# Kernel optimization log

Hardware: AMD Instinct MI355X
Metric: run time of the kernel (lower is better)

The kernel has to match this reference:

```python
import jax, jax.numpy as jnp
from jax import lax
import numpy as np

B = 2; C = 128; H = 128; W = 128; NPIX = H * W
HTH = 184; HTW = 180; NBINS = HTH * HTW
NSPH = 16384; KHT = 8; KSPH = 16
N0, N1, N2 = 1024, 256, 64
K0, K1, K2 = 8, 8, 8
EPS = 1e-5


def setup_inputs() -> dict:
    key = jax.random.key(0)
    ks = jax.random.split(key, 24)
    f32 = jnp.float32
    inp = {}
    inp["image"] = jax.random.normal(ks[0], (B, C, H, W), f32)
    inp["bn_gamma"] = jnp.ones((C,), f32)
    inp["bn_beta"] = jnp.zeros((C,), f32)
    inp["ht_idx"] = jax.random.randint(ks[1], (NBINS, KHT), 0, NPIX, jnp.int32)
    inp["ht_w"] = jax.random.uniform(ks[2], (NBINS, KHT), f32)
    inp["w_htconv"] = jax.random.normal(ks[3], (3, 3, C, C), f32) / np.sqrt(9.0 * C)
    inp["htbn_gamma"] = jnp.ones((C,), f32)
    inp["htbn_beta"] = jnp.zeros((C,), f32)
    inp["sph_idx"] = jax.random.randint(ks[4], (NSPH, KSPH), 0, NBINS, jnp.int32)
    inp["sph_w"] = jax.random.uniform(ks[5], (NSPH, KSPH), f32)
    inp["w_sc"] = jax.random.normal(ks[6], (3, 64, C), f32) / np.sqrt(1.0 * C)
    inp["b_sc"] = jnp.zeros((3, 64), f32)
    inp["scbn_gamma"] = jnp.ones((3, 64), f32)
    inp["scbn_beta"] = jnp.zeros((3, 64), f32)
    inp["dgcn_w"] = jax.random.normal(ks[7], (3, 4, 128, 64), f32) / np.sqrt(128.0)
    inp["dgcn_b"] = jnp.zeros((3, 4, 64), f32)
    inp["dgcn_hw"] = jax.random.normal(ks[8], (3, 64), f32) / 8.0
    inp["dgcn_hb"] = jnp.zeros((3,), f32)
    inp["ind0"] = jax.random.randint(ks[9], (B, N0), 0, NSPH, jnp.int32)
    inp["ind1"] = jax.random.randint(ks[10], (B, 3, N1), 0, NSPH, jnp.int32)
    inp["ind2"] = jax.random.randint(ks[11], (B, 3, N2), 0, NSPH, jnp.int32)
    # kNN-style edges: structured centers (each node repeated k times), random neighbors
    c0 = jnp.tile(jnp.repeat(jnp.arange(N0, dtype=jnp.int32), K0)[None], (B, 1))
    inp["edge0"] = jnp.stack([c0, jax.random.randint(ks[12], (B, N0 * K0), 0, N0, jnp.int32)], 1)
    c1 = jnp.broadcast_to(jnp.repeat(jnp.arange(N1, dtype=jnp.int32), K1)[None, None], (B, 3, N1 * K1))
    inp["edge1"] = jnp.stack([c1, jax.random.randint(ks[13], (B, 3, N1 * K1), 0, N1, jnp.int32)], 2)
    c2 = jnp.broadcast_to(jnp.repeat(jnp.arange(N2, dtype=jnp.int32), K2)[None, None], (B, 3, N2 * K2))
    inp["edge2"] = jnp.stack([c2, jax.random.randint(ks[14], (B, 3, N2 * K2), 0, N2, jnp.int32)], 2)
    inp["target0"] = jax.random.randint(ks[15], (B, N0), 0, 2, jnp.int32)
    inp["target1"] = jax.random.randint(ks[16], (B * 3, N1), 0, 2, jnp.int32)
    inp["target2"] = jax.random.randint(ks[17], (B * 3, N2), 0, 2, jnp.int32)
    return inp


def _bn2d(x, g, b):
    m = x.mean((0, 2, 3), keepdims=True)
    v = x.var((0, 2, 3), keepdims=True)
    return g[None, :, None, None] * (x - m) * lax.rsqrt(v + EPS) + b[None, :, None, None]


def _sphere(x_htf, sph_idx, sph_w, ind):
    # x_htf: [B,C,NBINS]; ind: [B,S] -> weighted gather of HT bins per sphere node
    mi = sph_idx[ind]          # [B,S,K]
    mw = sph_w[ind]            # [B,S,K]
    g = jax.vmap(lambda xb, ib: xb[:, ib])(x_htf, mi)   # [B,C,S,K]
    return (g * mw[:, None]).sum(-1)                    # [B,C,S]


def _sconv(x, w, b, g, be):
    # 1x1 conv [B,C,S]->[B,64,S] + BN1d (batch stats) + ReLU
    y = jnp.einsum('oc,bcs->bos', w, x) + b[None, :, None]
    m = y.mean((0, 2), keepdims=True)
    v = y.var((0, 2), keepdims=True)
    return jax.nn.relu(g[None, :, None] * (y - m) * lax.rsqrt(v + EPS) + be[None, :, None])


def _dgcn(x, edge, ws, bs, hw, hb, n, k):
    # x: [Bg,n,64]; edge: [Bg,2,n*k] (row0=center, row1=neighbor); 4 EdgeConv layers
    for i in range(4):
        xc = jnp.take_along_axis(x, edge[:, 0, :, None], axis=1)   # [Bg,n*k,Cin]
        xn = jnp.take_along_axis(x, edge[:, 1, :, None], axis=1)
        h = jax.nn.relu(jnp.concatenate([xc, xn - xc], -1) @ ws[i] + bs[i])
        x = h.reshape(x.shape[0], n, k, -1).max(2)                 # max over neighbors
    return x @ hw + hb                                             # [Bg,n] logits


def _bce(logits, target):
    t = target.astype(logits.dtype)
    l = jnp.maximum(logits, 0.0) - logits * t + jnp.log1p(jnp.exp(-jnp.abs(logits)))
    pos = t > 0.5
    npos = jnp.maximum(pos.sum(), 1).astype(l.dtype)
    nneg = jnp.maximum((~pos).sum(), 1).astype(l.dtype)
    return jnp.where(pos, l, 0.0).sum() / npos, jnp.where(pos, 0.0, l).sum() / nneg


def _forward(image, bn_gamma, bn_beta, ht_idx, ht_w, w_htconv, htbn_gamma, htbn_beta,
             sph_idx, sph_w, w_sc, b_sc, scbn_gamma, scbn_beta,
             dgcn_w, dgcn_b, dgcn_hw, dgcn_hb,
             ind0, ind1, ind2, edge0, edge1, edge2, target0, target1, target2):
    x = jax.nn.relu(_bn2d(image, bn_gamma, bn_beta))
    xf = x.reshape(B, C, NPIX)
    # Hough voting: each HT bin accumulates KHT weighted pixels
    ht = (xf[:, :, ht_idx] * ht_w).sum(-1).reshape(B, C, HTH, HTW)
    hc = lax.conv_general_dilated(ht, w_htconv, (1, 1), 'SAME',
                                  dimension_numbers=('NCHW', 'HWIO', 'NCHW'))
    x_htf = jax.nn.relu(_bn2d(hc, htbn_gamma, htbn_beta)).reshape(B, C, NBINS)

    # scale 0
    x0 = _sconv(_sphere(x_htf, sph_idx, sph_w, ind0),
                w_sc[0], b_sc[0], scbn_gamma[0], scbn_beta[0]).transpose(0, 2, 1)
    x0 = _dgcn(x0, edge0, dgcn_w[0], dgcn_b[0], dgcn_hw[0], dgcn_hb[0], N0, K0)   # [B,N0]
    # scale 1 (3 vanishing-point branches folded into batch)
    x1 = _sconv(_sphere(x_htf, sph_idx, sph_w, ind1.reshape(B, -1)),
                w_sc[1], b_sc[1], scbn_gamma[1], scbn_beta[1]).transpose(0, 2, 1)
    x1 = _dgcn(x1.reshape(B * 3, N1, 64), edge1.reshape(B * 3, 2, N1 * K1),
               dgcn_w[1], dgcn_b[1], dgcn_hw[1], dgcn_hb[1], N1, K1)              # [B*3,N1]
    # scale 2
    x2 = _sconv(_sphere(x_htf, sph_idx, sph_w, ind2.reshape(B, -1)),
                w_sc[2], b_sc[2], scbn_gamma[2], scbn_beta[2]).transpose(0, 2, 1)
    x2 = _dgcn(x2.reshape(B * 3, N2, 64), edge2.reshape(B * 3, 2, N2 * K2),
               dgcn_w[2], dgcn_b[2], dgcn_hw[2], dgcn_hb[2], N2, K2)              # [B*3,N2]

    lp0, ln0 = _bce(x0, target0)
    lp1, ln1 = _bce(x1, target1)
    lp2, ln2 = _bce(x2, target2)
    losses = jnp.stack([lp0, ln0, lp1, ln1, lp2, ln2])
    preds = jnp.concatenate([jax.nn.sigmoid(x0).reshape(B, -1),
                             jax.nn.sigmoid(x1).reshape(B, -1),
                             jax.nn.sigmoid(x2).reshape(B, -1)], axis=1)
    return losses, preds


def reference(image, bn_gamma, bn_beta, ht_idx, ht_w, w_htconv, htbn_gamma, htbn_beta,
              sph_idx, sph_w, w_sc, b_sc, scbn_gamma, scbn_beta,
              dgcn_w, dgcn_b, dgcn_hw, dgcn_hb,
              ind0, ind1, ind2, edge0, edge1, edge2, target0, target1, target2):
    return _forward(image, bn_gamma, bn_beta, ht_idx, ht_w, w_htconv, htbn_gamma, htbn_beta,
                    sph_idx, sph_w, w_sc, b_sc, scbn_gamma, scbn_beta,
                    dgcn_w, dgcn_b, dgcn_hw, dgcn_hb,
                    ind0, ind1, ind2, edge0, edge1, edge2, target0, target1, target2)
```

## Files before the change

kernel.cpp:

```cpp
#include <hip/hip_runtime.h>
#include <math.h>

#define B_ 2
#define C_ 128
#define NPIX_ 16384
#define HTH_ 184
#define HTW_ 180
#define NBINS_ 33120
#define PH_ 186
#define PW_ 184
#define NPB_ 1984
#define TOTN_ 3968
#define EPS_ 1e-5f

#define ST_HC_SUM 0
#define ST_HC_SQ  128
#define ST_SC_SUM 256
#define ST_SC_SQ  448
#define ST_LOSS   640
#define ST_IMG_S1 1472
#define ST_IMG_S2 1600

typedef __attribute__((ext_vector_type(8))) short v8s;
typedef __attribute__((ext_vector_type(4))) float v4f;

__device__ inline unsigned short f2b(float f) {
  unsigned u = __builtin_bit_cast(unsigned, f);
  unsigned r = u + 0x7fffu + ((u >> 16) & 1u);
  return (unsigned short)(r >> 16);
}
__device__ inline float b2f(unsigned short u) {
  unsigned v = ((unsigned)u) << 16;
  return __builtin_bit_cast(float, v);
}

__global__ void kprep0(const float* __restrict__ w, const float* __restrict__ dw,
                       const float* __restrict__ wsc,
                       unsigned short* __restrict__ wtb, unsigned short* __restrict__ dwb,
                       unsigned short* __restrict__ swb,
                       unsigned* __restrict__ htb2, const float* __restrict__ img,
                       float* __restrict__ st) {
  int bid = blockIdx.x;
  int tid = threadIdx.x;
  if (bid < 1612) {
    int idx = bid*256 + tid;
    if (idx < 147456) {
      int tap = idx >> 14, z = idx & 16383;
      int j = z & 7, lane = (z >> 3) & 63, nt = (z >> 9) & 7, kt = (z >> 12) & 3;
      int l = lane & 15, q = lane >> 4;
      int co = nt*16 + l, ci = kt*32 + q*8 + j;
      wtb[idx] = f2b(w[(tap*C_ + ci)*C_ + co]);
    } else if (idx < 245760) {
      int i2 = idx - 147456;
      int sl = i2 >> 13, z = i2 & 8191;
      int j = z & 7, lane = (z >> 3) & 63, nt = (z >> 9) & 3, kt = (z >> 11) & 3;
      int l = lane & 15, q = lane >> 4;
      int co = nt*16 + l, cc = kt*32 + q*8 + j;
      dwb[i2] = f2b(dw[(sl*128 + cc)*64 + co]);
    } else if (idx < 270336) {
      int i3 = idx - 245760;
      int s = i3 >> 13, z = i3 & 8191;
      int j = z & 7, lane = (z >> 3) & 63, nt = (z >> 9) & 3, kt = (z >> 11) & 3;
      int l = lane & 15, q = lane >> 4;
      int co = nt*16 + l, cc = kt*32 + q*8 + j;
      swb[i3] = f2b(wsc[(s*64 + co)*128 + cc]);
    } else if (idx < 412672) {
      int i = idx - 270336;
      int d = i & 63;
      int cell = i >> 6;
      int b = cell / 1112, j = cell % 1112;
      int y, x;
      if (j < 184) { y = 0; x = j; }
      else if (j < 368) { y = 185; x = j - 184; }
      else { int c = j - 368; int xi = c / 186; y = c % 186; x = xi == 0 ? 0 : 180 + xi; }
      htb2[((size_t)(b*PH_ + y)*PW_ + x)*64 + d] = 0u;
    }
  } else {
    int kb = bid - 1612;
    int c = kb >> 3, chunk = kb & 7;
    float s1 = 0.f, s2 = 0.f;
    for (int i = chunk*4096 + tid; i < (chunk+1)*4096; i += 256) {
      int b = i >> 14, p = i & (NPIX_-1);
      float v = img[((size_t)(b*C_ + c))*NPIX_ + p];
      s1 += v; s2 += v*v;
    }
    __shared__ float r1[256], r2[256];
    r1[tid] = s1; r2[tid] = s2; __syncthreads();
    for (int off = 128; off; off >>= 1) {
      if (tid < off) { r1[tid] += r1[tid+off]; r2[tid] += r2[tid+off]; }
      __syncthreads();
    }
    if (tid == 0) {
      atomicAdd(&st[ST_IMG_S1 + c], r1[0]);
      atomicAdd(&st[ST_IMG_S2 + c], r2[0]);
    }
  }
}

__global__ void k2_bnrelu_t(const float* __restrict__ img, const float* __restrict__ st,
                            const float* __restrict__ g, const float* __restrict__ be,
                            unsigned short* __restrict__ xt) {
  __shared__ float tile[32*65];
  __shared__ float ash[32], dsh[32];
  int p0 = blockIdx.x*64, c0 = blockIdx.y*32, b = blockIdx.z;
  int tid = threadIdx.x;
  if (tid < 32) {
    int c = c0 + tid;
    float n = (float)(B_*NPIX_);
    float m = st[ST_IMG_S1+c]/n;
    float var = st[ST_IMG_S2+c]/n - m*m;
    float a = g[c]*rsqrtf(var + EPS_);
    ash[tid] = a; dsh[tid] = be[c] - a*m;
  }
  __syncthreads();
  for (int r = 0; r < 8; r++) {
    int flat = tid + r*256;
    int row = flat >> 6, col = flat & 63;
    float v = img[((size_t)(b*C_ + c0 + row))*NPIX_ + p0 + col];
    tile[row*65 + col] = fmaxf(ash[row]*v + dsh[row], 0.f);
  }
  __syncthreads();
  for (int r = 0; r < 4; r++) {
    int flat = (tid + r*256)*2;
    int pl = flat >> 5, cl = flat & 31;
    unsigned lo = f2b(tile[cl*65 + pl]);
    unsigned hi = f2b(tile[(cl+1)*65 + pl]);
    *(unsigned*)&xt[((size_t)b*NPIX_ + p0 + pl)*C_ + c0 + cl] = lo | (hi << 16);
  }
}

__global__ void k3_hough(const unsigned* __restrict__ xt2, const int* __restrict__ hidx,
                         const float* __restrict__ hwt, unsigned* __restrict__ htb2) {
  int tid = threadIdx.x;
  int wv = __builtin_amdgcn_readfirstlane(tid >> 6);
  int bin = blockIdx.x*4 + wv;
  int b = blockIdx.y;
  int lane = tid & 63;
  const unsigned* base = xt2 + (size_t)b*NPIX_*64 + lane;
  float acc0 = 0.f, acc1 = 0.f;
  #pragma unroll
  for (int k = 0; k < 8; k++) {
    int p = hidx[bin*8 + k];
    float w = hwt[bin*8 + k];
    unsigned dv = base[(size_t)p*64];
    acc0 += w * b2f((unsigned short)(dv & 0xffff));
    acc1 += w * b2f((unsigned short)(dv >> 16));
  }
  int y = bin / HTW_, x = bin - y*HTW_;
  unsigned lo = f2b(acc0), hi = f2b(acc1);
  htb2[((size_t)(b*PH_ + y + 1)*PW_ + (x+1))*64 + lane] = lo | (hi << 16);
}

__global__ __launch_bounds__(256) void k4_mfma(
    const unsigned short* __restrict__ htb, const unsigned short* __restrict__ wtb,
    unsigned short* __restrict__ hcb, float* __restrict__ st) {
  __shared__ char smem[65536];
  int tid = threadIdx.x;
  int wav = tid >> 6, lane = tid & 63;
  int quad = lane >> 4, l16 = lane & 15;
  int b = blockIdx.y;
  int p0 = blockIdx.x*128 + wav*32;
  size_t ab[2];
  #pragma unroll
  for (int t = 0; t < 2; t++) {
    int px = p0 + t*16 + l16; if (px > NBINS_-1) px = NBINS_-1;
    int y = px / HTW_, x = px % HTW_;
    ab[t] = (((size_t)(b*PH_ + y))*PW_ + x)*C_ + quad*8;
  }
  v4f acc[2][8];
  #pragma unroll
  for (int t = 0; t < 2; t++)
    #pragma unroll
    for (int nt = 0; nt < 8; nt++) acc[t][nt] = (v4f){0,0,0,0};

  {
    const uint4* src = (const uint4*)wtb;
    uint4* dst = (uint4*)smem;
    #pragma unroll
    for (int s = 0; s < 8; s++) dst[tid + s*256] = src[tid + s*256];
  }
  __syncthreads();
  for (int tap = 0; tap < 9; tap++) {
    uint4 wreg[8];
    if (tap < 8) {
      const uint4* src = (const uint4*)(wtb + (tap+1)*16384);
      #pragma unroll
      for (int s = 0; s < 8; s++) wreg[s] = src[tid + s*256];
    }
    const char* cur = smem + (tap & 1)*32768;
    int dy = tap/3, dx = tap - dy*3;
    int toff = (dy*PW_ + dx)*C_;
    v8s a[2][4];
    #pragma unroll
    for (int t = 0; t < 2; t++)
      #pragma unroll
      for (int kt = 0; kt < 4; kt++)
        a[t][kt] = *(const v8s*)&htb[ab[t] + toff + kt*32];
    #pragma unroll
    for (int kt = 0; kt < 4; kt++) {
      #pragma unroll
      for (int nt = 0; nt < 8; nt++) {
        v8s bf = *(const v8s*)(cur + ((((kt*8 + nt)*64) + lane) << 4));
        acc[0][nt] = __builtin_amdgcn_mfma_f32_16x16x32_bf16(a[0][kt], bf, acc[0][nt], 0, 0, 0);
        acc[1][nt] = __builtin_amdgcn_mfma_f32_16x16x32_bf16(a[1][kt], bf, acc[1][nt], 0, 0, 0);
      }
    }
    if (tap < 8) {
      uint4* dst = (uint4*)(smem + ((tap+1) & 1)*32768);
      #pragma unroll
      for (int s = 0; s < 8; s++) dst[tid + s*256] = wreg[s];
    }
    __syncthreads();
  }
  float* red = (float*)smem;
  float s1[8], s2[8];
  #pragma unroll
  for (int nt = 0; nt < 8; nt++) { s1[nt] = 0.f; s2[nt] = 0.f; }
  #pragma unroll
  for (int t = 0; t < 2; t++) {
    int pbase = p0 + t*16 + quad*4;
    #pragma unroll
    for (int nt = 0; nt < 8; nt++) {
      int co = nt*16 + l16;
      #pragma unroll
      for (int reg = 0; reg < 4; reg++) {
        int po = pbase + reg;
        if (po < NBINS_) {
          float v = acc[t][nt][reg];
          hcb[((size_t)b*NBINS_ + po)*C_ + co] = f2b(v);
          s1[nt] += v; s2[nt] += v*v;
        }
      }
    }
  }
  int slot = wav*4 + quad;
  #pragma unroll
  for (int nt = 0; nt < 8; nt++) red[(nt*16 + l16)*17 + slot] = s1[nt];
  __syncthreads();
  if (tid < 128) {
    float s = 0.f;
    #pragma unroll
    for (int k = 0; k < 16; k++) s += red[tid*17 + k];
    atomicAdd(&st[ST_HC_SUM + tid], s);
  }
  __syncthreads();
  #pragma unroll
  for (int nt = 0; nt < 8; nt++) red[(nt*16 + l16)*17 + slot] = s2[nt];
  __syncthreads();
  if (tid < 128) {
    float s = 0.f;
    #pragma unroll
    for (int k = 0; k < 16; k++) s += red[tid*17 + k];
    atomicAdd(&st[ST_HC_SQ + tid], s);
  }
}

__global__ __launch_bounds__(256) void k67_sphconv(
    const unsigned* __restrict__ hcb2, const float* __restrict__ g, const float* __restrict__ be,
    const int* __restrict__ sph_idx, const float* __restrict__ sph_w,
    const int* __restrict__ ind0, const int* __restrict__ ind1, const int* __restrict__ ind2,
    const unsigned short* __restrict__ swb, const float* __restrict__ b_sc,
    float* __restrict__ y, float* __restrict__ st) {
  __shared__ unsigned short E[16*136];
  int tid = threadIdx.x;
  int gn0 = blockIdx.x*8;
  int nb0 = gn0 % NPB_;
  int s = nb0 < 1024 ? 0 : (nb0 < 1792 ? 1 : 2);
  int wv = tid >> 6, lane = tid & 63;
  int quad = lane >> 4, l16 = lane & 15;
  {
    int c0 = lane*2, c1 = c0 + 1;
    float n = (float)(B_*NBINS_);
    float m0 = st[ST_HC_SUM + c0]/n, m1 = st[ST_HC_SUM + c1]/n;
    float va0 = st[ST_HC_SQ + c0]/n - m0*m0, va1 = st[ST_HC_SQ + c1]/n - m1*m1;
    float a0 = g[c0]*rsqrtf(va0 + EPS_), a1 = g[c1]*rsqrtf(va1 + EPS_);
    float d0 = be[c0] - a0*m0, d1 = be[c1] - a1*m1;
    #pragma unroll
    for (int i = 0; i < 2; i++) {
      int node_l = wv*2 + i;
      int gn = gn0 + node_l;
      int b = gn / NPB_, nb = gn % NPB_;
      int v;
      if (nb < 1024) v = ind0[b*1024 + nb];
      else if (nb < 1792) v = ind1[b*768 + nb - 1024];
      else v = ind2[b*192 + nb - 1792];
      v = __builtin_amdgcn_readfirstlane(v);
      const unsigned* base = hcb2 + (size_t)b*NBINS_*64 + lane;
      float acc0 = 0.f, acc1 = 0.f;
      #pragma unroll
      for (int k = 0; k < 16; k++) {
        int mi = sph_idx[v*16 + k];
        float mw = sph_w[v*16 + k];
        unsigned dv = base[(size_t)mi*64];
        acc0 += mw * fmaxf(a0*b2f((unsigned short)(dv & 0xffff)) + d0, 0.f);
        acc1 += mw * fmaxf(a1*b2f((unsigned short)(dv >> 16)) + d1, 0.f);
      }
      unsigned lo = f2b(acc0), hi = f2b(acc1);
      *(unsigned*)&E[node_l*136 + c0] = lo | (hi << 16);
    }
  }
  __syncthreads();
  v4f acc = (v4f){0,0,0,0};
  const unsigned short* wb = swb + s*8192 + wv*512;
  #pragma unroll
  for (int kt = 0; kt < 4; kt++) {
    v8s a = *(const v8s*)&E[l16*136 + quad*8 + kt*32];
    v8s bf = *(const v8s*)&wb[kt*2048 + lane*8];
    acc = __builtin_amdgcn_mfma_f32_16x16x32_bf16(a, bf, acc, 0, 0, 0);
  }
  float bias = b_sc[s*64 + wv*16 + l16];
  float s1 = 0.f, s2 = 0.f;
  #pragma unroll
  for (int reg = 0; reg < 4; reg++) {
    int row = quad*4 + reg;
    if (quad < 2) {
      float val = acc[reg] + bias;
      y[(size_t)(gn0 + row)*64 + wv*16 + l16] = val;
      s1 += val; s2 += val*val;
    }
  }
  s1 += __shfl_xor(s1, 16);
  s2 += __shfl_xor(s2, 16);
  if (quad == 0) {
    atomicAdd(&st[ST_SC_SUM + s*64 + wv*16 + l16], s1);
    atomicAdd(&st[ST_SC_SQ  + s*64 + wv*16 + l16], s2);
  }
}

__global__ __launch_bounds__(256) void k10_dgcn(
    const void* __restrict__ xin_, unsigned short* __restrict__ xout,
    const int* __restrict__ edge0, const int* __restrict__ edge1, const int* __restrict__ edge2,
    const unsigned short* __restrict__ dwb, const float* __restrict__ db,
    const float* __restrict__ st, const float* __restrict__ scg, const float* __restrict__ scb,
    int layer, int usebn) {
  __shared__ unsigned short E[64*136];
  __shared__ float ash[64], dsh[64];
  int tid = threadIdx.x;
  int bid = blockIdx.x;
  int s, node_base, le_blk, span; const int* ec;
  if (bid < 256) {
    s = 0; int b = bid >> 7; node_base = b*NPB_; le_blk = (bid & 127)*64;
    span = 8192; ec = edge0 + b*2*8192;
  } else if (bid < 448) {
    int j = bid - 256; s = 1; int seg = j >> 5; int b = seg/3, vp = seg%3;
    node_base = b*NPB_ + 1024 + vp*256; le_blk = (j & 31)*64;
    span = 2048; ec = edge1 + ((b*3+vp)*2)*2048;
  } else {
    int j = bid - 448; s = 2; int seg = j >> 3; int b = seg/3, vp = seg%3;
    node_base = b*NPB_ + 1792 + vp*64; le_blk = (j & 7)*64;
    span = 512; ec = edge2 + ((b*3+vp)*2)*512;
  }
  const int* en = ec + span;
  if (usebn) {
    if (tid < 64) {
      float n = s==0 ? 2048.f : (s==1 ? 1536.f : 384.f);
      float m = st[ST_SC_SUM + s*64 + tid]/n;
      float var = st[ST_SC_SQ + s*64 + tid]/n - m*m;
      float a = scg[s*64 + tid]*rsqrtf(var + EPS_);
      ash[tid] = a; dsh[tid] = scb[s*64 + tid] - a*m;
    }
    __syncthreads();
  }
  {
    int e_l = tid >> 2, part = tid & 3;
    int h = part >> 1, cb = (part & 1)*32;
    int e = le_blk + e_l;
    int ci = ec[e], ni = en[e];
    if (usebn) {
      const float* xc = (const float*)xin_ + (size_t)(node_base + ci)*64 + cb;
      const float* xn = (const float*)xin_ + (size_t)(node_base + ni)*64 + cb;
      float4 xc4[8], xn4[8];
      #pragma unroll
      for (int q = 0; q < 8; q++) xc4[q] = *(const float4*)&xc[q*4];
      if (h) {
        #pragma unroll
        for (int q = 0; q < 8; q++) xn4[q] = *(const float4*)&xn[q*4];
      }
      #pragma unroll
      for (int c8 = 0; c8 < 32; c8 += 8) {
        v8s pk;
        #pragma unroll
        for (int j = 0; j < 8; j++) {
          int cl = c8 + j;
          int c = cb + cl;
          float xcv = ((const float*)xc4)[cl];
          float vc = fmaxf(ash[c]*xcv + dsh[c], 0.f);
          float val = vc;
          if (h) {
            float xnv = ((const float*)xn4)[cl];
            val = fmaxf(ash[c]*xnv + dsh[c], 0.f) - vc;
          }
          pk[j] = (short)f2b(val);
        }
        *(v8s*)&E[e_l*136 + h*64 + cb + c8] = pk;
      }
    } else {
      const unsigned short* xc = (const unsigned short*)xin_ + (size_t)(node_base + ci)*64 + cb;
      const unsigned short* xn = (const unsigned short*)xin_ + (size_t)(node_base + ni)*64 + cb;
      #pragma unroll
      for (int c8 = 0; c8 < 32; c8 += 8) {
        v8s vc8 = *(const v8s*)&xc[c8];
        v8s pk = vc8;
        if (h) {
          v8s vn8 = *(const v8s*)&xn[c8];
          #pragma unroll
          for (int j = 0; j < 8; j++)
            pk[j] = (short)f2b(b2f((unsigned short)vn8[j]) - b2f((unsigned short)vc8[j]));
        }
        *(v8s*)&E[e_l*136 + h*64 + cb + c8] = pk;
      }
    }
  }
  __syncthreads();
  int wave = tid >> 6, lane = tid & 63;
  int quad = lane >> 4, l16 = lane & 15;
  const unsigned short* wb = dwb + (size_t)(s*4 + layer)*8192;
  v4f acc[4];
  #pragma unroll
  for (int nt = 0; nt < 4; nt++) acc[nt] = (v4f){0,0,0,0};
  #pragma unroll
  for (int kt = 0; kt < 4; kt++) {
    v8s a = *(const v8s*)&E[(wave*16 + l16)*136 + quad*8 + kt*32];
    #pragma unroll
    for (int nt = 0; nt < 4; nt++) {
      v8s bf = *(const v8s*)&wb[((kt*4 + nt)*64 + lane)*8];
      acc[nt] = __builtin_amdgcn_mfma_f32_16x16x32_bf16(a, bf, acc[nt], 0, 0, 0);
    }
  }
  #pragma unroll
  for (int nt = 0; nt < 4; nt++) {
    float bias = db[(s*4 + layer)*64 + nt*16 + l16];
    float m = fmaxf(fmaxf(acc[nt][0], acc[nt][1]), fmaxf(acc[nt][2], acc[nt][3]));
    m = fmaxf(m + bias, 0.f);
    float other = __shfl_xor(m, 16);
    m = fmaxf(m, other);
    if ((quad & 1) == 0) {
      int node_l = wave*2 + (quad >> 1);
      xout[(size_t)(node_base + (le_blk >> 3) + node_l)*64 + nt*16 + l16] = f2b(m);
    }
  }
}

__global__ __launch_bounds__(256) void k11_head(
    const unsigned short* __restrict__ x, const float* __restrict__ hw, const float* __restrict__ hb,
    const int* __restrict__ t0, const int* __restrict__ t1, const int* __restrict__ t2,
    float* __restrict__ out, float* __restrict__ st) {
  __shared__ float shw[192];
  int tid = threadIdx.x;
  if (tid < 192) shw[tid] = hw[tid];
  __syncthreads();
  int gn = blockIdx.x*256 + tid;
  bool valid = gn < TOTN_;
  int g = valid ? gn : TOTN_-1;
  int b = g / NPB_, nb = g % NPB_;
  int s, tg;
  if (nb < 1024) { s = 0; tg = t0[b*1024 + nb]; }
  else if (nb < 1792) { s = 1; int j = nb-1024; tg = t1[(b*3 + (j>>8))*256 + (j&255)]; }
  else { s = 2; int j = nb-1792; tg = t2[(b*3 + (j>>6))*64 + (j&63)]; }
  const unsigned short* row = x + (size_t)g*64;
  float logit = hb[s];
  #pragma unroll
  for (int c8 = 0; c8 < 64; c8 += 8) {
    v8s v = *(const v8s*)&row[c8];
    #pragma unroll
    for (int j = 0; j < 8; j++)
      logit += b2f((unsigned short)v[j]) * shw[s*64 + c8 + j];
  }
  if (valid) out[6 + gn] = 1.f / (1.f + expf(-logit));
  float tf = (float)tg;
  float l = fmaxf(logit, 0.f) - logit*tf + log1pf(expf(-fabsf(logit)));
  float sp = (valid && tg) ? l : 0.f;
  float sn = (valid && !tg) ? l : 0.f;
  float cp = (valid && tg) ? 1.f : 0.f;
  float cn = (valid && !tg) ? 1.f : 0.f;
  for (int off = 32; off; off >>= 1) {
    sp += __shfl_down(sp, off);
    sn += __shfl_down(sn, off);
    cp += __shfl_down(cp, off);
    cn += __shfl_down(cn, off);
  }
  if ((tid & 63) == 0) {
    atomicAdd(&st[ST_LOSS + s*4 + 0], sp);
    atomicAdd(&st[ST_LOSS + s*4 + 1], sn);
    atomicAdd(&st[ST_LOSS + s*4 + 2], cp);
    atomicAdd(&st[ST_LOSS + s*4 + 3], cn);
  }
}

__global__ void k12_fin(const float* __restrict__ st, float* __restrict__ out) {
  int i = threadIdx.x;
  if (i < 6) {
    int s = i >> 1; int pos = !(i & 1);
    float sum = st[ST_LOSS + s*4 + (pos ? 0 : 1)];
    float cnt = st[ST_LOSS + s*4 + (pos ? 2 : 3)];
    out[i] = sum / fmaxf(cnt, 1.f);
  }
}

extern "C" void kernel_launch(void* const* d_in, const int* in_sizes, int n_in,
                              void* d_out, int out_size, void* d_ws, size_t ws_size,
                              hipStream_t stream) {
  const float* image  = (const float*)d_in[0];
  const float* bn_g   = (const float*)d_in[1];
  const float* bn_b   = (const float*)d_in[2];
  const int*   ht_idx = (const int*)  d_in[3];
  const float* ht_w   = (const float*)d_in[4];
  const float* w_conv = (const float*)d_in[5];
  const float* htbn_g = (const float*)d_in[6];
  const float* htbn_b = (const float*)d_in[7];
  const int*   sph_idx= (const int*)  d_in[8];
  const float* sph_w  = (const float*)d_in[9];
  const float* w_sc   = (const float*)d_in[10];
  const float* b_sc   = (const float*)d_in[11];
  const float* scbn_g = (const float*)d_in[12];
  const float* scbn_b = (const float*)d_in[13];
  const float* dgcn_w = (const float*)d_in[14];
  const float* dgcn_b = (const float*)d_in[15];
  const float* dgcn_hw= (const float*)d_in[16];
  const float* dgcn_hb= (const float*)d_in[17];
  const int*   ind0   = (const int*)  d_in[18];
  const int*   ind1   = (const int*)  d_in[19];
  const int*   ind2   = (const int*)  d_in[20];
  const int*   edge0  = (const int*)  d_in[21];
  const int*   edge1  = (const int*)  d_in[22];
  const int*   edge2  = (const int*)  d_in[23];
  const int*   t0     = (const int*)  d_in[24];
  const int*   t1     = (const int*)  d_in[25];
  const int*   t2     = (const int*)  d_in[26];
  float* out = (float*)d_out;

  char* ws = (char*)d_ws;
  unsigned short* x_t   = (unsigned short*)(ws);
  unsigned short* htb   = (unsigned short*)(ws +  8388608);
  unsigned short* hcb   = (unsigned short*)(ws + 25911296);
  unsigned short* wtb   = (unsigned short*)(ws + 42868736);
  unsigned short* dwb   = (unsigned short*)(ws + 43163648);
  unsigned short* swb   = (unsigned short*)(ws + 43360256);
  float*          y_sc  = (float*)(ws + 43409408);
  unsigned short* xdgA  = (unsigned short*)(ws + 44425216);
  unsigned short* xdgB  = (unsigned short*)(ws + 44933120);
  float*          st    = (float*)(ws + 45441024);

  hipMemsetAsync(st, 0, 1728*sizeof(float), stream);
  kprep0<<<2636, 256, 0, stream>>>(w_conv, dgcn_w, w_sc, wtb, dwb, swb, (unsigned*)htb, image, st);
  k2_bnrelu_t<<<dim3(256,4,2), 256, 0, stream>>>(image, st, bn_g, bn_b, x_t);
  k3_hough<<<dim3(NBINS_/4, B_), 256, 0, stream>>>((const unsigned*)x_t, ht_idx, ht_w, (unsigned*)htb);
  k4_mfma<<<dim3(259, 2), 256, 0, stream>>>(htb, wtb, hcb, st);
  k67_sphconv<<<TOTN_/8, 256, 0, stream>>>((const unsigned*)hcb, htbn_g, htbn_b, sph_idx, sph_w,
                                           ind0, ind1, ind2, swb, b_sc, y_sc, st);
  k10_dgcn<<<496, 256, 0, stream>>>((const void*)y_sc, xdgA, edge0, edge1, edge2, dwb, dgcn_b, st, scbn_g, scbn_b, 0, 1);
  k10_dgcn<<<496, 256, 0, stream>>>((const void*)xdgA, xdgB, edge0, edge1, edge2, dwb, dgcn_b, st, scbn_g, scbn_b, 1, 0);
  k10_dgcn<<<496, 256, 0, stream>>>((const void*)xdgB, xdgA, edge0, edge1, edge2, dwb, dgcn_b, st, scbn_g, scbn_b, 2, 0);
  k10_dgcn<<<496, 256, 0, stream>>>((const void*)xdgA, xdgB, edge0, edge1, edge2, dwb, dgcn_b, st, scbn_g, scbn_b, 3, 0);
  k11_head<<<16, 256, 0, stream>>>(xdgB, dgcn_hw, dgcn_hb, t0, t1, t2, out, st);
  k12_fin<<<1, 64, 0, stream>>>(st, out);
}
```

Baseline: 241.7 us.

## Batch Hough gathers, single-buffer conv weights, fuse loss finalize into head kernel

The Hough kernel now has each wave handle four bins, issuing all 32 gathers before accumulating, which raises memory-level parallelism and cuts the block count. The MFMA conv kernel drops the double-buffered weight tile, halving its LDS footprint, and adds a launch bound of 3 blocks per CU to allow higher occupancy, at the cost of exposing weight loads between taps behind barriers. The final loss-normalisation kernel is removed and replaced by a last-block ticket in the head kernel, which saves one launch but relies on a float atomic counter and threadfence ordering.

```diff
diff --git a/kernel.cpp b/kernel.cpp
--- a/kernel.cpp
+++ b/kernel.cpp
@@ -18,6 +18,7 @@
 #define ST_SC_SUM 256
 #define ST_SC_SQ  448
 #define ST_LOSS   640
+#define ST_TICKET 652
 #define ST_IMG_S1 1472
 #define ST_IMG_S2 1600
 
@@ -133,28 +134,39 @@
                          const float* __restrict__ hwt, unsigned* __restrict__ htb2) {
   int tid = threadIdx.x;
   int wv = __builtin_amdgcn_readfirstlane(tid >> 6);
-  int bin = blockIdx.x*4 + wv;
+  int lane = tid & 63;
   int b = blockIdx.y;
-  int lane = tid & 63;
+  int bin0 = blockIdx.x*16 + wv*4;
   const unsigned* base = xt2 + (size_t)b*NPIX_*64 + lane;
-  float acc0 = 0.f, acc1 = 0.f;
-  #pragma unroll
-  for (int k = 0; k < 8; k++) {
-    int p = hidx[bin*8 + k];
-    float w = hwt[bin*8 + k];
-    unsigned dv = base[(size_t)p*64];
-    acc0 += w * b2f((unsigned short)(dv & 0xffff));
-    acc1 += w * b2f((unsigned short)(dv >> 16));
-  }
-  int y = bin / HTW_, x = bin - y*HTW_;
-  unsigned lo = f2b(acc0), hi = f2b(acc1);
-  htb2[((size_t)(b*PH_ + y + 1)*PW_ + (x+1))*64 + lane] = lo | (hi << 16);
-}
-
-__global__ __launch_bounds__(256) void k4_mfma(
+  unsigned dv[4][8];
+  #pragma unroll
+  for (int i = 0; i < 4; i++) {
+    #pragma unroll
+    for (int k = 0; k < 8; k++) {
+      int p = hidx[(bin0+i)*8 + k];
+      dv[i][k] = base[(size_t)p*64];
+    }
+  }
+  #pragma unroll
+  for (int i = 0; i < 4; i++) {
+    int bin = bin0 + i;
+    float acc0 = 0.f, acc1 = 0.f;
+    #pragma unroll
+    for (int k = 0; k < 8; k++) {
+      float w = hwt[bin*8 + k];
+      acc0 += w * b2f((unsigned short)(dv[i][k] & 0xffff));
+      acc1 += w * b2f((unsigned short)(dv[i][k] >> 16));
+    }
+    int y = bin / HTW_, x = bin - y*HTW_;
+    htb2[((size_t)(b*PH_ + y + 1)*PW_ + (x+1))*64 + lane] =
+        (unsigned)f2b(acc0) | (((unsigned)f2b(acc1)) << 16);
+  }
+}
+
+__global__ __launch_bounds__(256, 3) void k4_mfma(
     const unsigned short* __restrict__ htb, const unsigned short* __restrict__ wtb,
     unsigned short* __restrict__ hcb, float* __restrict__ st) {
-  __shared__ char smem[65536];
+  __shared__ char smem[32768];
   int tid = threadIdx.x;
   int wav = tid >> 6, lane = tid & 63;
   int quad = lane >> 4, l16 = lane & 15;
@@ -173,21 +185,13 @@
     #pragma unroll
     for (int nt = 0; nt < 8; nt++) acc[t][nt] = (v4f){0,0,0,0};
 
-  {
-    const uint4* src = (const uint4*)wtb;
+  for (int tap = 0; tap < 9; tap++) {
+    __syncthreads();
+    const uint4* src = (const uint4*)(wtb + tap*16384);
     uint4* dst = (uint4*)smem;
     #pragma unroll
     for (int s = 0; s < 8; s++) dst[tid + s*256] = src[tid + s*256];
-  }
-  __syncthreads();
-  for (int tap = 0; tap < 9; tap++) {
-    uint4 wreg[8];
-    if (tap < 8) {
-      const uint4* src = (const uint4*)(wtb + (tap+1)*16384);
-      #pragma unroll
-      for (int s = 0; s < 8; s++) wreg[s] = src[tid + s*256];
-    }
-    const char* cur = smem + (tap & 1)*32768;
+    __syncthreads();
     int dy = tap/3, dx = tap - dy*3;
     int toff = (dy*PW_ + dx)*C_;
     v8s a[2][4];
@@ -200,18 +204,13 @@
     for (int kt = 0; kt < 4; kt++) {
       #pragma unroll
       for (int nt = 0; nt < 8; nt++) {
-        v8s bf = *(const v8s*)(cur + ((((kt*8 + nt)*64) + lane) << 4));
+        v8s bf = *(const v8s*)(smem + ((((kt*8 + nt)*64) + lane) << 4));
         acc[0][nt] = __builtin_amdgcn_mfma_f32_16x16x32_bf16(a[0][kt], bf, acc[0][nt], 0, 0, 0);
         acc[1][nt] = __builtin_amdgcn_mfma_f32_16x16x32_bf16(a[1][kt], bf, acc[1][nt], 0, 0, 0);
       }
     }
-    if (tap < 8) {
-      uint4* dst = (uint4*)(smem + ((tap+1) & 1)*32768);
-      #pragma unroll
-      for (int s = 0; s < 8; s++) dst[tid + s*256] = wreg[s];
-    }
-    __syncthreads();
-  }
+  }
+  __syncthreads();
   float* red = (float*)smem;
   float s1[8], s2[8];
   #pragma unroll
@@ -485,15 +484,19 @@
     atomicAdd(&st[ST_LOSS + s*4 + 2], cp);
     atomicAdd(&st[ST_LOSS + s*4 + 3], cn);
   }
-}
-
-__global__ void k12_fin(const float* __restrict__ st, float* __restrict__ out) {
-  int i = threadIdx.x;
-  if (i < 6) {
-    int s = i >> 1; int pos = !(i & 1);
-    float sum = st[ST_LOSS + s*4 + (pos ? 0 : 1)];
-    float cnt = st[ST_LOSS + s*4 + (pos ? 2 : 3)];
-    out[i] = sum / fmaxf(cnt, 1.f);
+  __syncthreads();
+  __threadfence();
+  if (tid == 0) {
+    unsigned t = (unsigned)atomicAdd(&st[ST_TICKET], 1.f);
+    if (t >= 15) {
+      #pragma unroll
+      for (int i = 0; i < 6; i++) {
+        int sc = i >> 1; int pos = !(i & 1);
+        float sum = atomicAdd(&st[ST_LOSS + sc*4 + (pos ? 0 : 1)], 0.f);
+        float cnt = atomicAdd(&st[ST_LOSS + sc*4 + (pos ? 2 : 3)], 0.f);
+        out[i] = sum / fmaxf(cnt, 1.f);
+      }
+    }
   }
 }
 
@@ -544,7 +547,7 @@
   hipMemsetAsync(st, 0, 1728*sizeof(float), stream);
   kprep0<<<2636, 256, 0, stream>>>(w_conv, dgcn_w, w_sc, wtb, dwb, swb, (unsigned*)htb, image, st);
   k2_bnrelu_t<<<dim3(256,4,2), 256, 0, stream>>>(image, st, bn_g, bn_b, x_t);
-  k3_hough<<<dim3(NBINS_/4, B_), 256, 0, stream>>>((const unsigned*)x_t, ht_idx, ht_w, (unsigned*)htb);
+  k3_hough<<<dim3(NBINS_/16, B_), 256, 0, stream>>>((const unsigned*)x_t, ht_idx, ht_w, (unsigned*)htb);
   k4_mfma<<<dim3(259, 2), 256, 0, stream>>>(htb, wtb, hcb, st);
   k67_sphconv<<<TOTN_/8, 256, 0, stream>>>((const unsigned*)hcb, htbn_g, htbn_b, sph_idx, sph_w,
                                            ind0, ind1, ind2, swb, b_sc, y_sc, st);
@@ -553,5 +556,4 @@
   k10_dgcn<<<496, 256, 0, stream>>>((const void*)xdgB, xdgA, edge0, edge1, edge2, dwb, dgcn_b, st, scbn_g, scbn_b, 2, 0);
   k10_dgcn<<<496, 256, 0, stream>>>((const void*)xdgA, xdgB, edge0, edge1, edge2, dwb, dgcn_b, st, scbn_g, scbn_b, 3, 0);
   k11_head<<<16, 256, 0, stream>>>(xdgB, dgcn_hw, dgcn_hb, t0, t1, t2, out, st);
-  k12_fin<<<1, 64, 0, stream>>>(st, out);
-}
+}
```

New measurement: 239.3 us. Within noise of the previous version (-1.0%).
